# Performance work log

Measured on AMD Instinct MI355X. Metric: run time of the kernel, lower is better.

## Reference

```python
import jax, jax.numpy as jnp
import numpy as np
import math

NUM_HEADS = 16
THETA = 10000.0

def setup_inputs() -> dict:
    key = jax.random.key(0)
    ks = jax.random.split(key, 5)
    B, S, D = 2, 2048, 1024
    sigma = math.sqrt(2.0 / (D + D))
    return {
        "x": jax.random.normal(ks[0], (B, S, D), dtype=jnp.float32),
        "token_positions": jnp.arange(B * S, dtype=jnp.int64 if jax.config.jax_enable_x64 else jnp.int32).reshape(B, S),
        "Wq": jax.random.normal(ks[1], (D, D), dtype=jnp.float32) * sigma,
        "Wk": jax.random.normal(ks[2], (D, D), dtype=jnp.float32) * sigma,
        "Wv": jax.random.normal(ks[3], (D, D), dtype=jnp.float32) * sigma,
        "Wo": jax.random.normal(ks[4], (D, D), dtype=jnp.float32) * sigma,
    }

def _rotate_half_interleaved(t):
    # pairs (x0,x1) -> (-x1, x0), interleaved layout as in the torch module
    *lead, d = t.shape
    t2 = t.reshape(*lead, d // 2, 2)
    r = jnp.stack([-t2[..., 1], t2[..., 0]], axis=-1)
    return r.reshape(*lead, d)

def reference(x, token_positions, Wq, Wk, Wv, Wo):
    B, S, D = x.shape
    H = NUM_HEADS
    hd = D // H

    # QKV projections (Linear stores weight as [out, in])
    q = (x @ Wq.T).reshape(B, S, H, hd).transpose(0, 2, 1, 3)  # [B,H,S,hd]
    k = (x @ Wk.T).reshape(B, S, H, hd).transpose(0, 2, 1, 3)
    v = (x @ Wv.T).reshape(B, S, H, hd).transpose(0, 2, 1, 3)

    # RoPE: inv_freq over even indices of head_dim
    inv_freq = 1.0 / (THETA ** (jnp.arange(0, hd, 2, dtype=jnp.float32) / hd))  # [hd/2]
    ang = token_positions.astype(jnp.float32)[..., None] * inv_freq  # [B,S,hd/2]
    cos = jnp.repeat(jnp.cos(ang), 2, axis=-1)[:, None]  # [B,1,S,hd]
    sin = jnp.repeat(jnp.sin(ang), 2, axis=-1)[:, None]
    q = q * cos + _rotate_half_interleaved(q) * sin
    k = k * cos + _rotate_half_interleaved(k) * sin

    # causal attention (full scores materialized, matching the torch module)
    scores = jnp.einsum('bhqd,bhkd->bhqk', q, k) / jnp.sqrt(jnp.float32(hd))
    causal = jnp.tril(jnp.ones((S, S), dtype=bool))
    scores = jnp.where(causal, scores, -jnp.inf)
    probs = jax.nn.softmax(scores, axis=-1)
    att = jnp.einsum('bhqk,bhkd->bhqd', probs, v)  # [B,H,S,hd]

    out = att.transpose(0, 2, 1, 3).reshape(B, S, D) @ Wo.T
    return out
```

## Files before the change

kernel.cpp:

```cpp
#include <hip/hip_runtime.h>
#include <hip/hip_bf16.h>

typedef __bf16 bf16;
typedef __bf16 bf16x4 __attribute__((ext_vector_type(4)));
typedef __bf16 bf16x8 __attribute__((ext_vector_type(8)));
typedef float f32x2 __attribute__((ext_vector_type(2)));
typedef float f32x4 __attribute__((ext_vector_type(4)));
typedef float f32x16 __attribute__((ext_vector_type(16)));
typedef unsigned int u32x4 __attribute__((ext_vector_type(4)));

#define NH 16
#define HD 64
#define SEQ 2048
#define DM 1024
#define MTOT 4096

__device__ __forceinline__ void gload_lds16(const void* g, void* l) {
  __builtin_amdgcn_global_load_lds(
      (const __attribute__((address_space(1))) void*)g,
      (__attribute__((address_space(3))) void*)l, 16, 0, 0);
}

__global__ __launch_bounds__(256) void prep_kernel(
    const float* __restrict__ x,
    const float* __restrict__ w0, const float* __restrict__ w1,
    const float* __restrict__ w2, const float* __restrict__ w3,
    const int* __restrict__ pos,
    bf16* __restrict__ xb, bf16* __restrict__ wb, float2* __restrict__ tab)
{
  int i = blockIdx.x * 256 + threadIdx.x;
  if (i < 1048576) {
    float4 v = reinterpret_cast<const float4*>(x)[i];
    bf16x4 o;
    o[0] = (bf16)v.x; o[1] = (bf16)v.y; o[2] = (bf16)v.z; o[3] = (bf16)v.w;
    *reinterpret_cast<bf16x4*>(xb + (size_t)i * 4) = o;
  } else if (i < 2097152) {
    int k = i - 1048576;
    int seg = k >> 18, j = k & 262143;
    const float* src = seg == 0 ? w0 : seg == 1 ? w1 : seg == 2 ? w2 : w3;
    float4 v = reinterpret_cast<const float4*>(src)[j];
    bf16x4 o;
    o[0] = (bf16)v.x; o[1] = (bf16)v.y; o[2] = (bf16)v.z; o[3] = (bf16)v.w;
    *reinterpret_cast<bf16x4*>(wb + ((size_t)seg << 20) + (size_t)j * 4) = o;
  } else if (i < 2097152 + 131072) {
    int k = i - 2097152;
    int m = k >> 5, i2 = k & 31;
    float pf = (float)pos[m];
    float inv = 1.0f / powf(10000.0f, (float)(2 * i2) * (1.0f / 64.0f));
    float a = pf * inv;
    tab[k] = make_float2(cosf(a), sinf(a));
  }
}

__global__ __launch_bounds__(512, 2) void gemm_qkv(
    const bf16* __restrict__ A, const bf16* __restrict__ wAll,
    bf16* __restrict__ outq, bf16* __restrict__ outk, bf16* __restrict__ outv,
    const float2* __restrict__ tab)
{
  __shared__ bf16 ABlds[2][2][2][8192];
  const int t = threadIdx.x;
  const int w = t >> 6;
  const int wm = w >> 2, wn = w & 3;
  const int lane = t & 63;
  const int lr = lane & 15;
  const int lg = lane >> 4;
  const int m0 = blockIdx.y * 256;
  const int proj = blockIdx.x >> 2;
  const int n0l = (blockIdx.x & 3) * 256;
  const char* Asrc = (const char*)A + (size_t)m0 * 2048;
  const char* Bsrc = (const char*)(wAll + ((size_t)proj << 20) + (size_t)n0l * DM);

  f32x4 acc[8][4] = {};
  bf16x8 bfr[4];

#define REG(AB_, PAR_, KK_) ((char*)ABlds + (((AB_)*4 + (PAR_)*2 + (KK_)) * 16384))

#define STAGE_HALF(AB_, T_, KK_)                                                   \
  {                                                                                \
    const char* gb_ = (AB_) ? Bsrc : Asrc;                                         \
    char* lb_ = REG(AB_, (T_) & 1, KK_);                                           \
    _Pragma("unroll")                                                              \
    for (int p_ = 0; p_ < 2; ++p_) {                                               \
      int o_ = (p_ * 512 + t) * 16;                                                \
      int r_ = o_ >> 6, c_ = o_ & 63;                                              \
      int cs_ = c_ ^ (((r_ >> 1) & 3) << 4);                                       \
      gload_lds16(gb_ + (size_t)r_ * 2048 + (T_) * 128 + (KK_) * 64 + cs_,         \
                  lb_ + o_);                                                       \
    }                                                                              \
  }

#define RDFRAG(DST, REGP, ROW)                                                     \
  {                                                                                \
    int row_ = (ROW);                                                              \
    int cb_ = (lg * 16) ^ (((row_ >> 1) & 3) << 4);                                \
    DST = *reinterpret_cast<const bf16x8*>((REGP) + row_ * 64 + cb_);              \
  }

#define PHASE(PAR, KK, MH, DOSTAGE, S_AB, S_T, S_KK, VM)                           \
  {                                                                                \
    bf16x8 af_[4];                                                                 \
    const char* areg_ = REG(0, PAR, KK);                                           \
    _Pragma("unroll")                                                              \
    for (int f_ = 0; f_ < 4; ++f_)                                                 \
      RDFRAG(af_[f_], areg_, wm * 128 + (MH) * 64 + f_ * 16 + lr);                 \
    if ((MH) == 0) {                                                               \
      const char* breg_ = REG(1, PAR, KK);                                         \
      _Pragma("unroll")                                                            \
      for (int j_ = 0; j_ < 4; ++j_)                                               \
        RDFRAG(bfr[j_], breg_, wn * 64 + j_ * 16 + lr);                            \
    }                                                                              \
    if (DOSTAGE) STAGE_HALF(S_AB, S_T, S_KK);                                      \
    if ((VM) == 8) asm volatile("s_waitcnt vmcnt(8)" ::: "memory");                \
    if ((VM) == 4) asm volatile("s_waitcnt vmcnt(4)" ::: "memory");                \
    if ((VM) == 0) asm volatile("s_waitcnt vmcnt(0)" ::: "memory");                \
    __builtin_amdgcn_sched_barrier(0);                                             \
    __builtin_amdgcn_s_barrier();                                                  \
    asm volatile("s_waitcnt lgkmcnt(0)" ::: "memory");                             \
    __builtin_amdgcn_sched_barrier(0);                                             \
    __builtin_amdgcn_s_setprio(1);                                                 \
    _Pragma("unroll")                                                              \
    for (int f_ = 0; f_ < 4; ++f_)                                                 \
      _Pragma("unroll")                                                            \
      for (int j_ = 0; j_ < 4; ++j_)                                               \
        acc[(MH) * 4 + f_][j_] = __builtin_amdgcn_mfma_f32_16x16x32_bf16(          \
            af_[f_], bfr[j_], acc[(MH) * 4 + f_][j_], 0, 0, 0);                    \
    __builtin_amdgcn_s_setprio(0);                                                 \
    __builtin_amdgcn_s_barrier();                                                  \
  }

  STAGE_HALF(0, 0, 0); STAGE_HALF(1, 0, 0);
  STAGE_HALF(0, 0, 1); STAGE_HALF(1, 0, 1);
  STAGE_HALF(0, 1, 0); STAGE_HALF(1, 1, 0);
  asm volatile("s_waitcnt vmcnt(4)" ::: "memory");
  __builtin_amdgcn_sched_barrier(0);
  __builtin_amdgcn_s_barrier();

  for (int i = 0; i < 7; ++i) {
    const int t1 = 2 * i + 1, t2 = 2 * i + 2, t3 = 2 * i + 3;
    PHASE(0, 0, 0, 1, 0, t1, 1, -1);
    PHASE(0, 0, 1, 1, 1, t1, 1,  8);
    PHASE(0, 1, 0, 1, 0, t2, 0, -1);
    PHASE(0, 1, 1, 1, 1, t2, 0,  8);
    PHASE(1, 0, 0, 1, 0, t2, 1, -1);
    PHASE(1, 0, 1, 1, 1, t2, 1,  8);
    PHASE(1, 1, 0, 1, 0, t3, 0, -1);
    PHASE(1, 1, 1, 1, 1, t3, 0,  8);
  }
  PHASE(0, 0, 0, 1, 0, 15, 1, -1);
  PHASE(0, 0, 1, 1, 1, 15, 1,  8);
  PHASE(0, 1, 0, 0, 0, 0, 0, -1);
  PHASE(0, 1, 1, 0, 0, 0, 0,  4);
  PHASE(1, 0, 0, 0, 0, 0, 0, -1);
  PHASE(1, 0, 1, 0, 0, 0, 0,  0);
  PHASE(1, 1, 0, 0, 0, 0, 0, -1);
  PHASE(1, 1, 1, 0, 0, 0, 0, -1);

#undef PHASE
#undef RDFRAG
#undef STAGE_HALF
#undef REG

  if (proj < 2) {
    bf16* outb = proj ? outk : outq;
#pragma unroll
    for (int j = 0; j < 4; ++j) {
      int nl = n0l + wn * 64 + j * 16 + lr;
      int h = nl >> 6, d = nl & 63;
      int i2 = d >> 1;
      bool odd = d & 1;
#pragma unroll
      for (int i = 0; i < 8; ++i) {
#pragma unroll
        for (int rr = 0; rr < 4; ++rr) {
          int m = m0 + wm * 128 + i * 16 + lg * 4 + rr;
          float v = acc[i][j][rr];
          float o = __shfl_xor(v, 1);
          float2 cs = tab[(m << 5) + i2];
          float res = odd ? (v * cs.x + o * cs.y) : (v * cs.x - o * cs.y);
          if (proj == 0) res *= 0.125f * 1.44269504f;
          outb[((size_t)((m >> 11) * NH + h) * SEQ + (m & 2047)) * HD + d] = (bf16)res;
        }
      }
    }
  } else {
#pragma unroll
    for (int j = 0; j < 4; ++j) {
      int nl = n0l + wn * 64 + j * 16 + lr;
      int h = nl >> 6, d = nl & 63;
#pragma unroll
      for (int i = 0; i < 8; ++i) {
#pragma unroll
        for (int rr = 0; rr < 4; ++rr) {
          int m = m0 + wm * 128 + i * 16 + lg * 4 + rr;
          outv[((size_t)((m >> 11) * NH + h) * HD + d) * SEQ + (m & 2047)] = (bf16)acc[i][j][rr];
        }
      }
    }
  }
}

__global__ __launch_bounds__(256) void gemm_out(
    const bf16* __restrict__ A, const bf16* __restrict__ Bw, float* __restrict__ outf)
{
  __shared__ bf16 As[2][128 * 32];
  __shared__ bf16 Bs[2][128 * 32];
  const int t = threadIdx.x;
  const int w = t >> 6;
  const int lane = t & 63;
  const int lr = lane & 15;
  const int lg = lane >> 4;
  const int m0 = blockIdx.y * 128;
  const int n0 = blockIdx.x * 128;
  const int wr = w >> 1, wc = w & 1;
  const char* Bb = (const char*)Bw;

  f32x4 acc[4][4] = {};

#define STAGE_OUT(KT, SLOT)                                                            \
  {                                                                                    \
    _Pragma("unroll")                                                                  \
    for (int p = 0; p < 2; ++p) {                                                      \
      int o = (p * 256 + t) * 16;                                                      \
      int r = o >> 6, cb = o & 63;                                                     \
      int m = m0 + r;                                                                  \
      const char* ga = (const char*)A +                                                \
          ((((size_t)(m >> 11) * NH + ((KT) >> 1)) * SEQ + (m & 2047)) * HD +          \
           ((KT) & 1) * 32) * 2 + cb;                                                  \
      gload_lds16(ga, (char*)As[SLOT] + o);                                            \
    }                                                                                  \
    _Pragma("unroll")                                                                  \
    for (int p = 0; p < 2; ++p) {                                                      \
      int o = (p * 256 + t) * 16;                                                      \
      int r = o >> 6, cb = o & 63;                                                     \
      gload_lds16(Bb + (size_t)(n0 + r) * 2048 + (KT) * 64 + cb, (char*)Bs[SLOT] + o); \
    }                                                                                  \
  }

  STAGE_OUT(0, 0);
  for (int kt = 0; kt < 32; ++kt) {
    asm volatile("s_waitcnt vmcnt(0)" ::: "memory");
    __builtin_amdgcn_sched_barrier(0);
    __builtin_amdgcn_s_barrier();
    if (kt + 1 < 32) STAGE_OUT(kt + 1, (kt + 1) & 1);

    const bf16* Abuf = As[kt & 1];
    const bf16* Bbuf = Bs[kt & 1];
    bf16x8 af[4], bfr[4];
#pragma unroll
    for (int f = 0; f < 4; ++f) {
      af[f]  = *reinterpret_cast<const bf16x8*>(Abuf + (wr * 64 + f * 16 + lr) * 32 + lg * 8);
      bfr[f] = *reinterpret_cast<const bf16x8*>(Bbuf + (wc * 64 + f * 16 + lr) * 32 + lg * 8);
    }
    __builtin_amdgcn_s_setprio(1);
#pragma unroll
    for (int i = 0; i < 4; ++i)
#pragma unroll
      for (int j = 0; j < 4; ++j)
        acc[i][j] = __builtin_amdgcn_mfma_f32_16x16x32_bf16(af[i], bfr[j], acc[i][j], 0, 0, 0);
    __builtin_amdgcn_s_setprio(0);
  }

#pragma unroll
  for (int j = 0; j < 4; ++j) {
    int n = n0 + wc * 64 + j * 16 + lr;
#pragma unroll
    for (int i = 0; i < 4; ++i) {
#pragma unroll
      for (int rr = 0; rr < 4; ++rr) {
        int m = m0 + wr * 64 + i * 16 + lg * 4 + rr;
        outf[(size_t)m * DM + n] = acc[i][j][rr];
      }
    }
  }
#undef STAGE_OUT
}

__device__ __forceinline__ void stage512(const char* gRow0, size_t rowStrideB, int colByte0,
                                         char* lds, int t) {
  int o = t * 16;
  int r = o >> 7;
  int cb = o & 127;
  int cbs = cb ^ ((r & 7) << 4);
  gload_lds16(gRow0 + (size_t)r * rowStrideB + colByte0 + cbs, lds + o);
}

__device__ __forceinline__ bf16x8 frag64(const char* tile, int row, int colByte) {
  int b = row * 128 + (colByte ^ ((row & 7) << 4));
  return *reinterpret_cast<const bf16x8*>(tile + b);
}

__device__ __forceinline__ unsigned packw(float a, float b) {
  unsigned short la = __builtin_bit_cast(unsigned short, (bf16)a);
  unsigned short lb = __builtin_bit_cast(unsigned short, (bf16)b);
  return (unsigned)la | ((unsigned)lb << 16);
}

__device__ __forceinline__ void plswap(unsigned& a, unsigned& b) {
  asm volatile("v_permlane32_swap_b32 %0, %1" : "+v"(a), "+v"(b));
}

__device__ __forceinline__ void tile_step(const char* Kt, const char* Vt,
                                          const bf16x8* qf,
                                          f32x16& acc0, f32x16& acc1,
                                          float& mrow, float& lrow,
                                          int l31, int h, bool domask, int qloc) {
  f32x16 s0 = {}, s1 = {};
  __builtin_amdgcn_s_setprio(1);
#pragma unroll
  for (int s = 0; s < 4; ++s) {
    bf16x8 kf0 = frag64(Kt, l31, s * 32 + h * 16);
    bf16x8 kf1 = frag64(Kt, 32 + l31, s * 32 + h * 16);
    s0 = __builtin_amdgcn_mfma_f32_32x32x16_bf16(kf0, qf[s], s0, 0, 0, 0);
    s1 = __builtin_amdgcn_mfma_f32_32x32x16_bf16(kf1, qf[s], s1, 0, 0, 0);
  }
  __builtin_amdgcn_s_setprio(0);
  if (domask) {
#pragma unroll
    for (int reg = 0; reg < 16; ++reg) {
      int ro = (reg & 3) + 8 * (reg >> 2) + 4 * h;
      if (ro > qloc) s0[reg] = -1e30f;
      if (ro + 32 > qloc) s1[reg] = -1e30f;
    }
  }
  float tm[16];
#pragma unroll
  for (int i = 0; i < 16; ++i) tm[i] = fmaxf(s0[i], s1[i]);
  float a0 = fmaxf(fmaxf(tm[0], tm[1]), tm[2]);
  float a1 = fmaxf(fmaxf(tm[3], tm[4]), tm[5]);
  float a2 = fmaxf(fmaxf(tm[6], tm[7]), tm[8]);
  float a3 = fmaxf(fmaxf(tm[9], tm[10]), tm[11]);
  float a4 = fmaxf(fmaxf(tm[12], tm[13]), tm[14]);
  float b0 = fmaxf(fmaxf(a0, a1), a2);
  float b1 = fmaxf(fmaxf(a3, a4), tm[15]);
  float tmax = fmaxf(b0, b1);
  float rmax = fmaxf(tmax, __shfl_xor(tmax, 32));

  bool need = __any(rmax > mrow + 11.5f);
  if (need) {
    float mnew = fmaxf(mrow, rmax);
    float osc = exp2f(mrow - mnew);
#pragma unroll
    for (int reg = 0; reg < 16; ++reg) {
      int rs = (reg & 3) + 8 * (reg >> 2) + 4 * h;
      float o = __shfl(osc, rs);
      acc0[reg] *= o;
      acc1[reg] *= o;
    }
    lrow *= osc;
    mrow = mnew;
  }
#pragma unroll
  for (int i = 0; i < 16; ++i) {
    s0[i] = exp2f(s0[i] - mrow);
    s1[i] = exp2f(s1[i] - mrow);
  }
  {
    const f32x2* p0 = reinterpret_cast<const f32x2*>(&s0);
    const f32x2* p1 = reinterpret_cast<const f32x2*>(&s1);
    f32x2 tp[8];
#pragma unroll
    for (int i = 0; i < 8; ++i) tp[i] = p0[i] + p1[i];
    tp[0] += tp[4]; tp[1] += tp[5]; tp[2] += tp[6]; tp[3] += tp[7];
    tp[0] += tp[2]; tp[1] += tp[3];
    tp[0] += tp[1];
    float rs = tp[0][0] + tp[0][1];
    lrow += rs + __shfl_xor(rs, 32);
  }

  unsigned W0[4][2], W1[4][2];
#pragma unroll
  for (int sp = 0; sp < 4; ++sp)
#pragma unroll
    for (int u = 0; u < 2; ++u) {
      W0[sp][u] = packw(s0[sp * 4 + 2 * u], s0[sp * 4 + 2 * u + 1]);
      W1[sp][u] = packw(s1[sp * 4 + 2 * u], s1[sp * 4 + 2 * u + 1]);
    }
  __builtin_amdgcn_s_setprio(1);
#pragma unroll
  for (int ks = 0; ks < 4; ++ks) {
    const unsigned (*W)[2] = (ks < 2) ? W0 : W1;
    const int c = ks & 1;
    unsigned a0w = W[2 * c][0], b0w = W[2 * c + 1][0];
    unsigned a1w = W[2 * c][1], b1w = W[2 * c + 1][1];
    plswap(a0w, b0w);
    plswap(a1w, b1w);
    u32x4 pw = {a0w, a1w, b0w, b1w};
    bf16x8 pf = __builtin_bit_cast(bf16x8, pw);
    bf16x8 vf0 = frag64(Vt, l31, ks * 32 + h * 16);
    bf16x8 vf1 = frag64(Vt, 32 + l31, ks * 32 + h * 16);
    acc0 = __builtin_amdgcn_mfma_f32_32x32x16_bf16(pf, vf0, acc0, 0, 0, 0);
    acc1 = __builtin_amdgcn_mfma_f32_32x32x16_bf16(pf, vf1, acc1, 0, 0, 0);
  }
  __builtin_amdgcn_s_setprio(0);
}

__global__ __launch_bounds__(512, 4) void attn_kernel(
    const bf16* __restrict__ q, const bf16* __restrict__ k,
    const bf16* __restrict__ vt, bf16* __restrict__ att)
{
  __shared__ __align__(16) char pool[65536];
  const int t = threadIdx.x;
  const int w = t >> 6;
  const int wsub = w & 3;
  const int par = w >> 2;
  const int lane = t & 63;
  const int l31 = lane & 31;
  const int h = lane >> 5;

  const int id = blockIdx.x;
  const int bh = (id & 7) + 8 * ((id >> 3) & 3);
  const int rem = id >> 5;
  const int halfb = rem >> 3;
  const int jj = rem & 7;
  const int j = halfb ? jj : 15 - jj;

  const int strip = 2 * j + (wsub >> 1);
  const int myN = strip + 1;
  const int npair = j + 1;
  const int q0w = j * 128 + wsub * 32;
  const int qloc = (wsub & 1) * 32 + l31;

  const bf16* qb = q + (size_t)bh * SEQ * HD;
  const char* kbB = (const char*)(k + (size_t)bh * SEQ * HD);
  const char* vbB = (const char*)(vt + (size_t)bh * HD * SEQ);

  bf16x8 qf[4];
#pragma unroll
  for (int s = 0; s < 4; ++s)
    qf[s] = *reinterpret_cast<const bf16x8*>(qb + (size_t)(q0w + l31) * HD + s * 16 + h * 8);

  f32x16 acc0 = {}, acc1 = {};
  float mrow = -1e30f, lrow = 0.f;

  stage512(kbB, 128, 0, pool + 0 * 8192, t);
  stage512(vbB, 4096, 0, pool + 32768 + 0 * 8192, t);
  stage512(kbB + 8192, 128, 0, pool + 1 * 8192, t);
  stage512(vbB, 4096, 128, pool + 32768 + 1 * 8192, t);

  for (int u = 0; u < npair; ++u) {
    asm volatile("s_waitcnt vmcnt(0)" ::: "memory");
    __builtin_amdgcn_sched_barrier(0);
    __builtin_amdgcn_s_barrier();
    if (u + 1 < npair) {
      int nt = 2 * u + 2;
      stage512(kbB + (size_t)nt * 8192, 128, 0, pool + (nt & 3) * 8192, t);
      stage512(vbB, 4096, nt * 128, pool + 32768 + (nt & 3) * 8192, t);
      stage512(kbB + (size_t)(nt + 1) * 8192, 128, 0, pool + ((nt + 1) & 3) * 8192, t);
      stage512(vbB, 4096, (nt + 1) * 128, pool + 32768 + ((nt + 1) & 3) * 8192, t);
    }
    const int tt = 2 * u + par;
    if (tt < myN)
      tile_step(pool + (tt & 3) * 8192, pool + 32768 + (tt & 3) * 8192, qf,
                acc0, acc1, mrow, lrow, l31, h, tt == strip, qloc);
  }

  __syncthreads();

  float* mb = (float*)pool;
  float* reg = mb + wsub * (34 * 64);
  if (par == 1) {
#pragma unroll
    for (int i = 0; i < 16; ++i) reg[i * 64 + lane] = acc0[i];
#pragma unroll
    for (int i = 0; i < 16; ++i) reg[(16 + i) * 64 + lane] = acc1[i];
    reg[32 * 64 + lane] = mrow;
    reg[33 * 64 + lane] = lrow;
  }
  __syncthreads();
  if (par == 0) {
    float mB = reg[32 * 64 + lane];
    float lB = reg[33 * 64 + lane];
    float mM = fmaxf(mrow, mB);
    float alpha = exp2f(mrow - mM);
    float beta  = exp2f(mB - mM);
    float linv = 1.0f / (alpha * lrow + beta * lB);
#pragma unroll
    for (int rg = 0; rg < 16; ++rg) {
      int rs = (rg & 3) + 8 * (rg >> 2) + 4 * h;
      float a  = __shfl(alpha, rs);
      float b  = __shfl(beta, rs);
      float li = __shfl(linv, rs);
      float o0 = (a * acc0[rg] + b * reg[rg * 64 + lane]) * li;
      float o1 = (a * acc1[rg] + b * reg[(16 + rg) * 64 + lane]) * li;
      size_t base = ((size_t)bh * SEQ + q0w + rs) * HD;
      att[base + l31]      = (bf16)o0;
      att[base + 32 + l31] = (bf16)o1;
    }
  }
}

extern "C" void kernel_launch(void* const* d_in, const int* in_sizes, int n_in,
                              void* d_out, int out_size, void* d_ws, size_t ws_size,
                              hipStream_t stream) {
  const float* x  = (const float*)d_in[0];
  const int* pos  = (const int*)d_in[1];
  const float* Wq = (const float*)d_in[2];
  const float* Wk = (const float*)d_in[3];
  const float* Wv = (const float*)d_in[4];
  const float* Wo = (const float*)d_in[5];
  float* out = (float*)d_out;

  char* p = (char*)d_ws;
  bf16* xb   = (bf16*)p; p += (size_t)MTOT * DM * 2;
  bf16* wqb  = (bf16*)p; p += (size_t)DM * DM * 2;
  bf16* wkb  = (bf16*)p; p += (size_t)DM * DM * 2;
  bf16* wvb  = (bf16*)p; p += (size_t)DM * DM * 2;
  bf16* wob  = (bf16*)p; p += (size_t)DM * DM * 2;
  bf16* qb   = (bf16*)p; p += (size_t)MTOT * DM * 2;
  bf16* kb   = (bf16*)p; p += (size_t)MTOT * DM * 2;
  bf16* vtb  = (bf16*)p; p += (size_t)MTOT * DM * 2;
  bf16* attb = (bf16*)p; p += (size_t)MTOT * DM * 2;
  float2* tab = (float2*)p; p += (size_t)MTOT * 32 * sizeof(float2);
  (void)wkb; (void)wvb;

  prep_kernel<<<(2097152 + 131072 + 255) / 256, 256, 0, stream>>>(
      x, Wq, Wk, Wv, Wo, pos, xb, wqb, tab);

  gemm_qkv<<<dim3(12, MTOT / 256), 512, 0, stream>>>(xb, wqb, qb, kb, vtb, tab);

  attn_kernel<<<512, 512, 0, stream>>>(qb, kb, vtb, attb);

  gemm_out<<<dim3(DM / 128, MTOT / 128), 256, 0, stream>>>(attb, wob, out);
}
```

Before: 119.2 us.

## Split long causal attention rows across two blocks and merge partials

Query tiles with long causal key ranges (j>=8) are split into two halves of their key-tile pairs, each processed by a separate block, so the grid grows from 512 to 768 blocks and the longest per-block work shrinks. Each split block writes unnormalized bf16 partial outputs plus per-row max and sum into scratch reused from the bf16 x buffer and the RoPE table. A new merge kernel combines the two partials with the log-sum-exp rescale and writes the final attention output. The aim is to cut the critical path from load imbalance in causal attention. The cost is an extra kernel launch, extra global traffic for the partials, and some precision loss from storing unnormalized partials in bf16.

```diff
diff --git a/kernel.cpp b/kernel.cpp
--- a/kernel.cpp
+++ b/kernel.cpp
@@ -396,7 +396,8 @@
 
 __global__ __launch_bounds__(512, 4) void attn_kernel(
     const bf16* __restrict__ q, const bf16* __restrict__ k,
-    const bf16* __restrict__ vt, bf16* __restrict__ att)
+    const bf16* __restrict__ vt, bf16* __restrict__ att,
+    bf16* __restrict__ accP, float* __restrict__ mP, float* __restrict__ lP)
 {
   __shared__ __align__(16) char pool[65536];
   const int t = threadIdx.x;
@@ -408,15 +409,25 @@
   const int h = lane >> 5;
 
   const int id = blockIdx.x;
-  const int bh = (id & 7) + 8 * ((id >> 3) & 3);
-  const int rem = id >> 5;
-  const int halfb = rem >> 3;
-  const int jj = rem & 7;
-  const int j = halfb ? jj : 15 - jj;
+  const int bh = id & 31;
+  const int unit = 23 - (id >> 5);
+  int j, u0, u1, pidx = 0;
+  bool partial;
+  if (unit < 8) {
+    j = unit; u0 = 0; u1 = j + 1; partial = false;
+  } else {
+    int v = unit - 8;
+    j = 8 + (v >> 1);
+    int ch = v & 1;
+    int h0 = (j + 1) >> 1;
+    u0 = ch ? h0 : 0;
+    u1 = ch ? (j + 1) : h0;
+    partial = true;
+    pidx = (bh * 8 + (j - 8)) * 2 + ch;
+  }
 
   const int strip = 2 * j + (wsub >> 1);
   const int myN = strip + 1;
-  const int npair = j + 1;
   const int q0w = j * 128 + wsub * 32;
   const int qloc = (wsub & 1) * 32 + l31;
 
@@ -432,16 +443,19 @@
   f32x16 acc0 = {}, acc1 = {};
   float mrow = -1e30f, lrow = 0.f;
 
-  stage512(kbB, 128, 0, pool + 0 * 8192, t);
-  stage512(vbB, 4096, 0, pool + 32768 + 0 * 8192, t);
-  stage512(kbB + 8192, 128, 0, pool + 1 * 8192, t);
-  stage512(vbB, 4096, 128, pool + 32768 + 1 * 8192, t);
-
-  for (int u = 0; u < npair; ++u) {
+  {
+    int pt = 2 * u0;
+    stage512(kbB + (size_t)pt * 8192, 128, 0, pool + (pt & 3) * 8192, t);
+    stage512(vbB, 4096, pt * 128, pool + 32768 + (pt & 3) * 8192, t);
+    stage512(kbB + (size_t)(pt + 1) * 8192, 128, 0, pool + ((pt + 1) & 3) * 8192, t);
+    stage512(vbB, 4096, (pt + 1) * 128, pool + 32768 + ((pt + 1) & 3) * 8192, t);
+  }
+
+  for (int u = u0; u < u1; ++u) {
     asm volatile("s_waitcnt vmcnt(0)" ::: "memory");
     __builtin_amdgcn_sched_barrier(0);
     __builtin_amdgcn_s_barrier();
-    if (u + 1 < npair) {
+    if (u + 1 < u1) {
       int nt = 2 * u + 2;
       stage512(kbB + (size_t)nt * 8192, 128, 0, pool + (nt & 3) * 8192, t);
       stage512(vbB, 4096, nt * 128, pool + 32768 + (nt & 3) * 8192, t);
@@ -473,20 +487,59 @@
     float mM = fmaxf(mrow, mB);
     float alpha = exp2f(mrow - mM);
     float beta  = exp2f(mB - mM);
-    float linv = 1.0f / (alpha * lrow + beta * lB);
-#pragma unroll
-    for (int rg = 0; rg < 16; ++rg) {
-      int rs = (rg & 3) + 8 * (rg >> 2) + 4 * h;
-      float a  = __shfl(alpha, rs);
-      float b  = __shfl(beta, rs);
-      float li = __shfl(linv, rs);
-      float o0 = (a * acc0[rg] + b * reg[rg * 64 + lane]) * li;
-      float o1 = (a * acc1[rg] + b * reg[(16 + rg) * 64 + lane]) * li;
-      size_t base = ((size_t)bh * SEQ + q0w + rs) * HD;
-      att[base + l31]      = (bf16)o0;
-      att[base + 32 + l31] = (bf16)o1;
-    }
-  }
+    if (!partial) {
+      float linv = 1.0f / (alpha * lrow + beta * lB);
+#pragma unroll
+      for (int rg = 0; rg < 16; ++rg) {
+        int rs = (rg & 3) + 8 * (rg >> 2) + 4 * h;
+        float a  = __shfl(alpha, rs);
+        float b  = __shfl(beta, rs);
+        float li = __shfl(linv, rs);
+        float o0 = (a * acc0[rg] + b * reg[rg * 64 + lane]) * li;
+        float o1 = (a * acc1[rg] + b * reg[(16 + rg) * 64 + lane]) * li;
+        size_t base = ((size_t)bh * SEQ + q0w + rs) * HD;
+        att[base + l31]      = (bf16)o0;
+        att[base + 32 + l31] = (bf16)o1;
+      }
+    } else {
+      float lC = alpha * lrow + beta * lB;
+      if (h == 0) {
+        mP[pidx * 128 + wsub * 32 + l31] = mM;
+        lP[pidx * 128 + wsub * 32 + l31] = lC;
+      }
+#pragma unroll
+      for (int rg = 0; rg < 16; ++rg) {
+        int rs = (rg & 3) + 8 * (rg >> 2) + 4 * h;
+        float a = __shfl(alpha, rs);
+        float b = __shfl(beta, rs);
+        float c0 = a * acc0[rg] + b * reg[rg * 64 + lane];
+        float c1 = a * acc1[rg] + b * reg[(16 + rg) * 64 + lane];
+        size_t base = (size_t)pidx * 8192 + (size_t)(wsub * 32 + rs) * 64;
+        accP[base + l31]      = (bf16)c0;
+        accP[base + 32 + l31] = (bf16)c1;
+      }
+    }
+  }
+}
+
+__global__ __launch_bounds__(256) void attn_merge(
+    const bf16* __restrict__ accP, const float* __restrict__ mP,
+    const float* __restrict__ lP, bf16* __restrict__ att)
+{
+  int gid = blockIdx.x * 256 + threadIdx.x;
+  int c = gid & 63;
+  int r = (gid >> 6) & 127;
+  int j8 = (gid >> 13) & 7;
+  int bh = gid >> 16;
+  int p0 = (bh * 8 + j8) * 2;
+  float m0 = mP[p0 * 128 + r], m1 = mP[(p0 + 1) * 128 + r];
+  float l0 = lP[p0 * 128 + r], l1 = lP[(p0 + 1) * 128 + r];
+  float a0 = (float)accP[(size_t)p0 * 8192 + r * 64 + c];
+  float a1 = (float)accP[(size_t)(p0 + 1) * 8192 + r * 64 + c];
+  float mM = fmaxf(m0, m1);
+  float e0 = exp2f(m0 - mM), e1 = exp2f(m1 - mM);
+  float o = (e0 * a0 + e1 * a1) / (e0 * l0 + e1 * l1);
+  att[((size_t)bh * SEQ + (8 + j8) * 128 + r) * HD + c] = (bf16)o;
 }
 
 extern "C" void kernel_launch(void* const* d_in, const int* in_sizes, int n_in,
@@ -513,12 +566,18 @@
   float2* tab = (float2*)p; p += (size_t)MTOT * 32 * sizeof(float2);
   (void)wkb; (void)wvb;
 
+  bf16* accP = xb;
+  float* mP = (float*)tab;
+  float* lP = mP + 512 * 128;
+
   prep_kernel<<<(2097152 + 131072 + 255) / 256, 256, 0, stream>>>(
       x, Wq, Wk, Wv, Wo, pos, xb, wqb, tab);
 
   gemm_qkv<<<dim3(12, MTOT / 256), 512, 0, stream>>>(xb, wqb, qb, kb, vtb, tab);
 
-  attn_kernel<<<512, 512, 0, stream>>>(qb, kb, vtb, attb);
+  attn_kernel<<<768, 512, 0, stream>>>(qb, kb, vtb, attb, accP, mP, lP);
+
+  attn_merge<<<8192, 256, 0, stream>>>(accP, mP, lP, attb);
 
   gemm_out<<<dim3(DM / 128, MTOT / 128), 256, 0, stream>>>(attb, wob, out);
 }
```

Result: slower. 125.7 us (+5.4%).
